# Performance work log

Measured on AMD Instinct MI355X. Metric: run time of the kernel, lower is better.

## Reference

```python
import jax, jax.numpy as jnp
import numpy as np

B, H, W, C, N = 4, 64, 2650, 64, 680000
THR = 0.5  # model_cfg.FOREGROUND_THRESHOLD


def setup_inputs() -> dict:
    key = jax.random.key(0)
    k1, k2, k3, k4, k5, k6 = jax.random.split(key, 6)
    pts = jax.random.normal(k1, (N, 5), dtype=jnp.float32)
    bidx = jax.random.randint(k2, (N,), 0, B)
    points = pts.at[:, 0].set(bidx.astype(jnp.float32))  # col 0 = batch index
    ri_h = jax.random.randint(k3, (N, 1), 0, H)
    ri_w = jax.random.randint(k4, (N, 1), 0, W)
    ri_indices = jnp.concatenate([ri_h, ri_w], axis=1).astype(jnp.int32)
    seg_pred = jax.random.uniform(k5, (B, H, W), dtype=jnp.float32)
    range_features = jax.random.normal(k6, (B, C, H, W), dtype=jnp.float32)
    return {"points": points, "ri_indices": ri_indices,
            "seg_pred": seg_pred, "range_features": range_features}


def reference(points, ri_indices, seg_pred, range_features):
    # Fully-vectorized version of the per-batch loop: each point gathers its
    # range-image feature/seg score via a flat (b*H*W + r*W + c) index.
    Bn, Cc, Hh, Ww = range_features.shape
    feats_flat = jnp.transpose(range_features, (0, 2, 3, 1)).reshape(Bn * Hh * Ww, Cc)
    seg_flat = seg_pred.reshape(Bn * Hh * Ww)
    b = points[:, 0].astype(jnp.int32)
    flat_idx = b * (Hh * Ww) + ri_indices[:, 0].astype(jnp.int32) * Ww + ri_indices[:, 1].astype(jnp.int32)  # [N]
    mask = seg_flat[flat_idx] >= THR                    # foreground mask [N] bool
    point_feats = feats_flat[flat_idx]                  # [N, C] gather
    out = jnp.concatenate([points, point_feats], axis=1)  # [N, 5+C]
    # jit-compatible stand-in for boolean compaction: zero out background rows
    out = out * mask[:, None].astype(out.dtype)
    return out, mask
```

## Files before the change

### kernel.cpp

```cpp
#include <hip/hip_runtime.h>

#define B_   4
#define H_   64
#define W_   2650
#define C_   64
#define N_   680000
#define THR_ 0.5f
#define HW_  (H_ * W_)
#define W16_ 166
#define M2_  (B_ * H_ * W16_)
#define NB2_ (M2_ / 256)


__global__ void zero_out_kernel(float4* __restrict__ p) {
    const size_t total = (size_t)N_ * 70 / 4;
    size_t i = (size_t)blockIdx.x * 256 + threadIdx.x;
    const size_t stride = (size_t)gridDim.x * 256;
    const float4 z = {0.f, 0.f, 0.f, 0.f};
    for (; i < total; i += stride) p[i] = z;
}

__global__ void zero_kernel(int* __restrict__ p) {
    p[blockIdx.x * 256 + threadIdx.x] = 0;
}

__global__ void hist_kernel(const float* __restrict__ pts,
                            const int* __restrict__ ri,
                            const float* __restrict__ seg,
                            int* __restrict__ binarr) {
    int i = blockIdx.x * 256 + threadIdx.x;
    if (i >= N_) return;
    int b = (int)pts[(size_t)i * 5];
    int2 rc = ((const int2*)ri)[i];
    if (seg[(size_t)b * HW_ + rc.x * W_ + rc.y] >= THR_)
        atomicAdd(&binarr[(b * H_ + rc.x) * W16_ + (rc.y >> 4)], 1);
}

__global__ void scan1_kernel(int* __restrict__ binarr, int* __restrict__ bsum) {
    __shared__ int lds[256];
    int t = threadIdx.x;
    int g = blockIdx.x * 256 + t;
    int v = binarr[g];
    lds[t] = v;
    __syncthreads();
    for (int off = 1; off < 256; off <<= 1) {
        int x = (t >= off) ? lds[t - off] : 0;
        __syncthreads();
        lds[t] += x;
        __syncthreads();
    }
    binarr[g] = lds[t] - v;
    if (t == 255) bsum[blockIdx.x] = lds[255];
}

__global__ void scan2_kernel(int* __restrict__ bsum) {
    __shared__ int lds[256];
    int t = threadIdx.x;
    int v = (t < NB2_) ? bsum[t] : 0;
    lds[t] = v;
    __syncthreads();
    for (int off = 1; off < 256; off <<= 1) {
        int x = (t >= off) ? lds[t - off] : 0;
        __syncthreads();
        lds[t] += x;
        __syncthreads();
    }
    if (t < NB2_) bsum[t] = lds[t] - v;
}

__global__ void scan3_kernel(int* __restrict__ binarr, const int* __restrict__ bsum) {
    int g = blockIdx.x * 256 + threadIdx.x;
    binarr[g] += bsum[blockIdx.x];
}

__global__ void scatter_kernel(const float* __restrict__ pts,
                               const int* __restrict__ ri,
                               const float* __restrict__ seg,
                               int* __restrict__ binarr,
                               int* __restrict__ perm) {
    int i = blockIdx.x * 256 + threadIdx.x;
    if (i >= N_) return;
    int b   = (int)pts[(size_t)i * 5];
    int2 rc = ((const int2*)ri)[i];
    int r = rc.x, c = rc.y;
    if (seg[(size_t)b * HW_ + r * W_ + c] < THR_) return;
    int bin  = (b * H_ + r) * W16_ + (c >> 4);
    int slot = atomicAdd(&binarr[bin], 1);
    perm[slot] = i | ((c & 15) << 20);
}

__global__ __launch_bounds__(256) void gather_kernel(
    const float* __restrict__ pts,
    const float* __restrict__ feat,
    const int*   __restrict__ binarr,
    const int*   __restrict__ perm,
    float* __restrict__ out,
    float* __restrict__ mask_out)
{
    __shared__ float lds[4][64 * 17];
    __shared__ float alds[4][64 * 5];
    const int lane  = threadIdx.x & 63;
    const int wslot = threadIdx.x >> 6;
    const int bin   = blockIdx.x * 4 + wslot;

    const int end   = binarr[bin];
    const int start = (bin == 0) ? 0 : binarr[bin - 1];
    if (start == end) return;

    const int b    = bin / (H_ * W16_);
    const int rem  = bin % (H_ * W16_);
    const int r    = rem / W16_;
    const int col0 = (rem % W16_) * 16;

    int cnt = min(end - start, 64);
    int rec_l = (lane < cnt) ? perm[start + lane] : 0;

    const size_t fbase = (size_t)(b * C_ + lane) * HW_ + (size_t)r * W_ + col0;
    float* dst = &lds[wslot][lane * 17];
    if (col0 + 16 <= W_) {
        const float2* s2 = (const float2*)(feat + fbase);
#pragma unroll
        for (int j = 0; j < 8; j++) {
            float2 v = s2[j];
            dst[2 * j] = v.x;
            dst[2 * j + 1] = v.y;
        }
    } else {
#pragma unroll
        for (int j = 0; j < 16; j++) {
            int col = col0 + j;
            if (col >= W_) col = W_ - 1;
            dst[j] = feat[(size_t)(b * C_ + lane) * HW_ + (size_t)r * W_ + col];
        }
    }

    float* arow = alds[wslot];
    int p0 = start;
    for (;;) {
        const int na = cnt * 5;
        for (int rbase = 0; rbase < na; rbase += 64) {
            int idx = rbase + lane;
            int pj  = idx / 5;
            int a   = idx - pj * 5;
            int pjc = (idx < na) ? pj : 0;
            int ptj = __shfl(rec_l, pjc) & 0xFFFFF;
            if (idx < na) arow[idx] = pts[(size_t)ptj * 5 + a];
        }
#pragma unroll 4
        for (int j = 0; j < cnt; j++) {
            const int rec = __shfl(rec_l, j);
            const int pt  = rec & 0xFFFFF;
            const float f = dst[(rec >> 20) & 15];
            const size_t orow = (size_t)pt * 69;
            out[orow + 5 + lane] = f;
            if (lane < 5) out[orow + lane] = arow[j * 5 + lane];
            if (lane == 0) mask_out[pt] = 1.0f;
        }
        p0 += cnt;
        if (p0 >= end) break;
        cnt = min(end - p0, 64);
        rec_l = (lane < cnt) ? perm[p0 + lane] : 0;
    }
}

__global__ __launch_bounds__(256) void gather_fallback(
    const float* __restrict__ pts, const int* __restrict__ ri,
    const float* __restrict__ seg, const float* __restrict__ feat,
    float* __restrict__ out, float* __restrict__ mask_out)
{
    const int lane = threadIdx.x & 63;
    const int pt   = blockIdx.x * 4 + (threadIdx.x >> 6);
    if (pt >= N_) return;
    int b = (int)pts[(size_t)pt * 5];
    int r = ri[pt * 2], c = ri[pt * 2 + 1];
    int rc = r * W_ + c;
    float m = (seg[b * HW_ + rc] >= THR_) ? 1.0f : 0.0f;
    float f = feat[(size_t)b * (C_ * HW_) + (size_t)lane * HW_ + rc];
    size_t orow = (size_t)pt * 69;
    out[orow + 5 + lane] = f * m;
    if (lane < 5) out[orow + lane] = pts[(size_t)pt * 5 + lane] * m;
    if (lane == 0) mask_out[pt] = m;
}


extern "C" void kernel_launch(void* const* d_in, const int* in_sizes, int n_in,
                              void* d_out, int out_size, void* d_ws, size_t ws_size,
                              hipStream_t stream) {
    const float* points = (const float*)d_in[0];
    const int*   ri     = (const int*)  d_in[1];
    const float* seg    = (const float*)d_in[2];
    const float* feat   = (const float*)d_in[3];

    float* out      = (float*)d_out;
    float* mask_out = (float*)d_out + (size_t)N_ * 69;

    int* binarr = (int*)d_ws;
    int* bsum   = binarr + M2_;
    int* perm   = bsum + 256;
    const size_t needed = ((size_t)M2_ + 256 + N_) * sizeof(int);
    const bool use_sort = (ws_size >= needed);

    const int nblkN = (N_ + 255) / 256;

    if (use_sort) {
        zero_out_kernel<<<2048,  256, 0, stream>>>((float4*)out);
        zero_kernel   <<<NB2_,   256, 0, stream>>>(binarr);
        hist_kernel   <<<nblkN,  256, 0, stream>>>(points, ri, seg, binarr);
        scan1_kernel  <<<NB2_,   256, 0, stream>>>(binarr, bsum);
        scan2_kernel  <<<1,      256, 0, stream>>>(bsum);
        scan3_kernel  <<<NB2_,   256, 0, stream>>>(binarr, bsum);
        scatter_kernel<<<nblkN,  256, 0, stream>>>(points, ri, seg, binarr, perm);
        gather_kernel <<<M2_ / 4, 256, 0, stream>>>(points, feat, binarr, perm,
                                                    out, mask_out);
    } else {
        gather_fallback<<<(N_ + 3) / 4, 256, 0, stream>>>(points, ri, seg, feat,
                                                          out, mask_out);
    }
}
```

Before: 429.5 us.

## Gather over 128-column strips per block and fuse zeroing kernels

The gather kernel now gives each block a 128-column strip of one row. The block stages all 64 channels of that strip into a shared LDS tile, and the strip's points are split evenly across its four waves. Before, each wave handled a single 16-column bin. The aim is wider coalesced feature loads, fewer tiny blocks, and better load balance. The two zeroing kernels are also merged into one launch. The cost is a larger LDS footprint per block, which lowers occupancy, plus an added block barrier.

```diff
diff --git a/kernel.cpp b/kernel.cpp
--- a/kernel.cpp
+++ b/kernel.cpp
@@ -10,18 +10,23 @@
 #define W16_ 166
 #define M2_  (B_ * H_ * W16_)
 #define NB2_ (M2_ / 256)
-
-
-__global__ void zero_out_kernel(float4* __restrict__ p) {
+#define SPR_ 21
+#define NSTRIP_ (B_ * H_ * SPR_)
+#define ROWF_ 129
+
+
+__global__ void zero_fused_kernel(int* __restrict__ binarr,
+                                  float4* __restrict__ outp) {
+    const int bid = blockIdx.x;
+    if (bid < NB2_) {
+        binarr[bid * 256 + threadIdx.x] = 0;
+        return;
+    }
     const size_t total = (size_t)N_ * 70 / 4;
-    size_t i = (size_t)blockIdx.x * 256 + threadIdx.x;
-    const size_t stride = (size_t)gridDim.x * 256;
+    size_t i = (size_t)(bid - NB2_) * 256 + threadIdx.x;
+    const size_t stride = (size_t)(gridDim.x - NB2_) * 256;
     const float4 z = {0.f, 0.f, 0.f, 0.f};
-    for (; i < total; i += stride) p[i] = z;
-}
-
-__global__ void zero_kernel(int* __restrict__ p) {
-    p[blockIdx.x * 256 + threadIdx.x] = 0;
+    for (; i < total; i += stride) outp[i] = z;
 }
 
 __global__ void hist_kernel(const float* __restrict__ pts,
@@ -86,7 +91,7 @@
     if (seg[(size_t)b * HW_ + r * W_ + c] < THR_) return;
     int bin  = (b * H_ + r) * W16_ + (c >> 4);
     int slot = atomicAdd(&binarr[bin], 1);
-    perm[slot] = i | ((c & 15) << 20);
+    perm[slot] = i | ((c & 127) << 20);
 }
 
 __global__ __launch_bounds__(256) void gather_kernel(
@@ -97,45 +102,61 @@
     float* __restrict__ out,
     float* __restrict__ mask_out)
 {
-    __shared__ float lds[4][64 * 17];
+    __shared__ float flds[64 * ROWF_];
     __shared__ float alds[4][64 * 5];
-    const int lane  = threadIdx.x & 63;
-    const int wslot = threadIdx.x >> 6;
-    const int bin   = blockIdx.x * 4 + wslot;
-
-    const int end   = binarr[bin];
-    const int start = (bin == 0) ? 0 : binarr[bin - 1];
+    const int t    = threadIdx.x;
+    const int lane = t & 63;
+    const int w    = t >> 6;
+
+    const int sx  = blockIdx.x % SPR_;
+    const int tmp = blockIdx.x / SPR_;
+    const int r   = tmp & (H_ - 1);
+    const int b   = tmp >> 6;
+
+    const int rowbin  = (b * H_ + r) * W16_;
+    const int first   = rowbin + sx * 8;
+    const int lastbin = rowbin + min(sx * 8 + 8, W16_) - 1;
+    const int start   = (first == 0) ? 0 : binarr[first - 1];
+    const int end     = binarr[lastbin];
     if (start == end) return;
 
-    const int b    = bin / (H_ * W16_);
-    const int rem  = bin % (H_ * W16_);
-    const int r    = rem / W16_;
-    const int col0 = (rem % W16_) * 16;
-
-    int cnt = min(end - start, 64);
-    int rec_l = (lane < cnt) ? perm[start + lane] : 0;
-
-    const size_t fbase = (size_t)(b * C_ + lane) * HW_ + (size_t)r * W_ + col0;
-    float* dst = &lds[wslot][lane * 17];
-    if (col0 + 16 <= W_) {
-        const float2* s2 = (const float2*)(feat + fbase);
+    const int tot = end - start;
+    const int q = tot >> 2, rm = tot & 3;
+    const int wstart = start + w * q + min(w, rm);
+    const int wend   = wstart + q + (w < rm ? 1 : 0);
+
+    int cnt = min(wend - wstart, 64);
+    int rec_l = (lane < cnt) ? perm[wstart + lane] : 0;
+
+    const int c0 = sx * 128;
+    if (c0 + 128 <= W_) {
 #pragma unroll
-        for (int j = 0; j < 8; j++) {
-            float2 v = s2[j];
-            dst[2 * j] = v.x;
-            dst[2 * j + 1] = v.y;
+        for (int g = 0; g < 16; g++) {
+            const int ch = 4 * g + w;
+            const int x  = 2 * (lane);
+            const float2 v = *(const float2*)(feat + (size_t)(b * C_ + ch) * HW_
+                                              + (size_t)r * W_ + c0 + x);
+            flds[ch * ROWF_ + x]     = v.x;
+            flds[ch * ROWF_ + x + 1] = v.y;
         }
     } else {
 #pragma unroll
-        for (int j = 0; j < 16; j++) {
-            int col = col0 + j;
-            if (col >= W_) col = W_ - 1;
-            dst[j] = feat[(size_t)(b * C_ + lane) * HW_ + (size_t)r * W_ + col];
-        }
-    }
-
-    float* arow = alds[wslot];
-    int p0 = start;
+        for (int g = 0; g < 16; g++) {
+            const int ch = 4 * g + w;
+            const int x  = 2 * (lane);
+            int c1 = c0 + x;     if (c1 >= W_) c1 = W_ - 1;
+            int c2 = c0 + x + 1; if (c2 >= W_) c2 = W_ - 1;
+            const size_t base = (size_t)(b * C_ + ch) * HW_ + (size_t)r * W_;
+            flds[ch * ROWF_ + x]     = feat[base + c1];
+            flds[ch * ROWF_ + x + 1] = feat[base + c2];
+        }
+    }
+    __syncthreads();
+    if (wstart >= wend) return;
+
+    float* arow = alds[w];
+    const float* myrow = &flds[lane * ROWF_];
+    int p0 = wstart;
     for (;;) {
         const int na = cnt * 5;
         for (int rbase = 0; rbase < na; rbase += 64) {
@@ -150,15 +171,15 @@
         for (int j = 0; j < cnt; j++) {
             const int rec = __shfl(rec_l, j);
             const int pt  = rec & 0xFFFFF;
-            const float f = dst[(rec >> 20) & 15];
+            const float f = myrow[(rec >> 20) & 127];
             const size_t orow = (size_t)pt * 69;
             out[orow + 5 + lane] = f;
             if (lane < 5) out[orow + lane] = arow[j * 5 + lane];
             if (lane == 0) mask_out[pt] = 1.0f;
         }
         p0 += cnt;
-        if (p0 >= end) break;
-        cnt = min(end - p0, 64);
+        if (p0 >= wend) break;
+        cnt = min(wend - p0, 64);
         rec_l = (lane < cnt) ? perm[p0 + lane] : 0;
     }
 }
@@ -203,14 +224,13 @@
     const int nblkN = (N_ + 255) / 256;
 
     if (use_sort) {
-        zero_out_kernel<<<2048,  256, 0, stream>>>((float4*)out);
-        zero_kernel   <<<NB2_,   256, 0, stream>>>(binarr);
+        zero_fused_kernel<<<NB2_ + 2048, 256, 0, stream>>>(binarr, (float4*)out);
         hist_kernel   <<<nblkN,  256, 0, stream>>>(points, ri, seg, binarr);
         scan1_kernel  <<<NB2_,   256, 0, stream>>>(binarr, bsum);
         scan2_kernel  <<<1,      256, 0, stream>>>(bsum);
         scan3_kernel  <<<NB2_,   256, 0, stream>>>(binarr, bsum);
         scatter_kernel<<<nblkN,  256, 0, stream>>>(points, ri, seg, binarr, perm);
-        gather_kernel <<<M2_ / 4, 256, 0, stream>>>(points, feat, binarr, perm,
+        gather_kernel <<<NSTRIP_, 256, 0, stream>>>(points, feat, binarr, perm,
                                                     out, mask_out);
     } else {
         gather_fallback<<<(N_ + 3) / 4, 256, 0, stream>>>(points, ri, seg, feat,
```

After: 417.8 us. -2.7%, faster.
